# Performance work log

Hardware: AMD Instinct MI355X
Metric: run time of the kernel (lower is better)

Reference implementation:

```python
import jax, jax.numpy as jnp
import numpy as np

N = 50000   # nnodes
E = 1600000 # edges (avg degree 32)
F = 128     # nfeatures
D = 64      # output_dim
T = 10      # s2v iterations (default in n2v)


def setup_inputs() -> dict:
    key = jax.random.key(0)
    k_x, k_s, k_d, k_w1, k_w2 = jax.random.split(key, 5)
    x = jax.random.normal(k_x, (N, F), dtype=jnp.float32)
    edge_src = jax.random.randint(k_s, (E,), 0, N, dtype=jnp.int32)
    edge_dst = jax.random.randint(k_d, (E,), 0, N, dtype=jnp.int32)
    # xavier_uniform init as in reset_parameters
    s1 = float(np.sqrt(6.0 / (F + D)))
    s2 = float(np.sqrt(6.0 / (D + D)))
    W1 = jax.random.uniform(k_w1, (D, F), jnp.float32, -s1, s1)
    W2 = jax.random.uniform(k_w2, (D, D), jnp.float32, -s2, s2)
    b1 = jnp.zeros((D,), jnp.float32)
    b2 = jnp.zeros((D,), jnp.float32)
    return {"x": x, "W1": W1, "b1": b1, "W2": W2, "b2": b2,
            "edge_src": edge_src, "edge_dst": edge_dst}


def reference(x, W1, b1, W2, b2, edge_src, edge_dst):
    Wx = x @ W1.T + b1                      # [N, D]

    def step(emb, _):
        # sum of neighbor embeddings: gather sources, segment-sum into dests
        agg = jax.ops.segment_sum(emb[edge_src], edge_dst, num_segments=N)  # [N, D]
        emb_new = jax.nn.relu(Wx + agg @ W2.T + b2)
        return emb_new, None

    emb0 = jnp.zeros((N, D), dtype=x.dtype)
    emb, _ = jax.lax.scan(step, emb0, None, length=T)  # n2v
    # g2v: sum node embeddings into graph embedding
    return emb.sum(axis=0)                  # [D]
```

## Files before the change

kernel.cpp:

```cpp
#include <hip/hip_runtime.h>

#define D 64
#define F 128
#define NBMAX 256

typedef unsigned int uint;
typedef unsigned short ushort;
typedef short s16x8 __attribute__((ext_vector_type(8)));
typedef float f32x4 __attribute__((ext_vector_type(4)));

__device__ __forceinline__ float bf16lo(uint u) { return __uint_as_float(u << 16); }
__device__ __forceinline__ float bf16hi(uint u) { return __uint_as_float(u & 0xFFFF0000u); }
__device__ __forceinline__ ushort f2bf16(float f) {
    uint u = __float_as_uint(f);
    u += 0x7FFFu + ((u >> 16) & 1u);
    return (ushort)(u >> 16);
}
__device__ __forceinline__ uint pk2bf(float lo, float hi) {
    return (uint)f2bf16(lo) | ((uint)f2bf16(hi) << 16);
}
__device__ __forceinline__ float rdlane(float v, int l) {
    return __uint_as_float(__builtin_amdgcn_readlane(__float_as_uint(v), l));
}


__global__ __launch_bounds__(256) void bucket_hist(const int* __restrict__ dst,
                                                   int* __restrict__ gb, int E, int nb) {
    __shared__ int h[NBMAX];
    for (int t = threadIdx.x; t < nb; t += 256) h[t] = 0;
    __syncthreads();
    int start = blockIdx.x * 4096;
    int end   = start + 4096 < E ? start + 4096 : E;
    for (int i = start + threadIdx.x; i < end; i += 256)
        atomicAdd(&h[dst[i] >> 8], 1);
    __syncthreads();
    for (int t = threadIdx.x; t < nb; t += 256)
        if (h[t]) atomicAdd(&gb[t], h[t]);
}

__global__ void bucket_scan(const int* __restrict__ gb, int* __restrict__ gboff,
                            int* __restrict__ gcur, int nb) {
    if (threadIdx.x == 0) {
        int s = 0;
        for (int b = 0; b < nb; ++b) { gboff[b] = s; gcur[b] = s; s += gb[b]; }
        gboff[nb] = s;
    }
}

__global__ __launch_bounds__(256) void bucket_scatter(const int* __restrict__ src,
                                                      const int* __restrict__ dst,
                                                      int* __restrict__ gcur,
                                                      int* __restrict__ packed, int E, int nb) {
    __shared__ int h[NBMAX], base[NBMAX], lcur[NBMAX];
    for (int t = threadIdx.x; t < nb; t += 256) h[t] = 0;
    __syncthreads();
    int start = blockIdx.x * 4096;
    int end   = start + 4096 < E ? start + 4096 : E;
    for (int i = start + threadIdx.x; i < end; i += 256)
        atomicAdd(&h[dst[i] >> 8], 1);
    __syncthreads();
    for (int t = threadIdx.x; t < nb; t += 256) {
        base[t] = h[t] ? atomicAdd(&gcur[t], h[t]) : 0;
        lcur[t] = 0;
    }
    __syncthreads();
    for (int i = start + threadIdx.x; i < end; i += 256) {
        int d = dst[i];
        int b = d >> 8;
        int pos = base[b] + atomicAdd(&lcur[b], 1);
        packed[pos] = (src[i] << 8) | (d & 255);
    }
}

__global__ __launch_bounds__(256) void bucket_deg(const int* __restrict__ gboff,
                                                  const int* __restrict__ packed,
                                                  int* __restrict__ deg, int N) {
    __shared__ int h[NBMAX];
    int b = blockIdx.x;
    h[threadIdx.x] = 0;
    __syncthreads();
    int st = gboff[b], en = gboff[b + 1];
    for (int i = st + threadIdx.x; i < en; i += 256)
        atomicAdd(&h[packed[i] & 255], 1);
    __syncthreads();
    int node = (b << 8) + threadIdx.x;
    if (node < N) deg[node] = h[threadIdx.x];
}

__global__ __launch_bounds__(256) void bucket_fill(const int* __restrict__ gboff,
                                                   const int* __restrict__ packed,
                                                   const int* __restrict__ row_ptr,
                                                   int* __restrict__ col, int N) {
    __shared__ int lcur[NBMAX];
    int b = blockIdx.x;
    int node = (b << 8) + threadIdx.x;
    lcur[threadIdx.x] = (node < N) ? row_ptr[node] : 0;
    __syncthreads();
    int st = gboff[b], en = gboff[b + 1];
    for (int i = st + threadIdx.x; i < en; i += 256) {
        int p = packed[i];
        int pos = atomicAdd(&lcur[p & 255], 1);
        col[pos] = p >> 8;
    }
}


__global__ void count_deg_kernel(const int* __restrict__ dst, int* __restrict__ deg, int E) {
    int i = blockIdx.x * blockDim.x + threadIdx.x;
    if (i < E) atomicAdd(&deg[dst[i]], 1);
}

__global__ void fill_kernel(const int* __restrict__ src, const int* __restrict__ dst,
                            int* __restrict__ cursor, int* __restrict__ col, int E) {
    int i = blockIdx.x * blockDim.x + threadIdx.x;
    if (i < E) {
        int d_ = dst[i];
        int pos = atomicAdd(&cursor[d_], 1);
        col[pos] = src[i];
    }
}


__global__ __launch_bounds__(1024) void scan_kernel(const int* __restrict__ deg,
                                                    int* __restrict__ row_ptr, int n) {
    __shared__ int wsum[16];
    int lane = threadIdx.x & 63;
    int wid  = threadIdx.x >> 6;
    int carry = 0;
    const int CH = 4096;
    for (int base = 0; base < n; base += CH) {
        int i0 = base + (int)threadIdx.x * 4;
        int v0 = (i0     < n) ? ((deg[i0]     + 15) & ~15) : 0;
        int v1 = (i0 + 1 < n) ? ((deg[i0 + 1] + 15) & ~15) : 0;
        int v2 = (i0 + 2 < n) ? ((deg[i0 + 2] + 15) & ~15) : 0;
        int v3 = (i0 + 3 < n) ? ((deg[i0 + 3] + 15) & ~15) : 0;
        int p0 = v0, p1 = p0 + v1, p2 = p1 + v2, p3 = p2 + v3;
        int tsum = p3;
        int s = tsum;
        #pragma unroll
        for (int off = 1; off < 64; off <<= 1) {
            int t = __shfl_up(s, off);
            if (lane >= off) s += t;
        }
        if (lane == 63) wsum[wid] = s;
        __syncthreads();
        int wbase = 0, chunk_total = 0;
        #pragma unroll
        for (int w = 0; w < 16; ++w) {
            int t = wsum[w];
            chunk_total += t;
            if (w < wid) wbase += t;
        }
        __syncthreads();
        int ex = carry + wbase + (s - tsum);
        if (i0     < n) row_ptr[i0 + 1] = ex + p0;
        if (i0 + 1 < n) row_ptr[i0 + 2] = ex + p1;
        if (i0 + 2 < n) row_ptr[i0 + 3] = ex + p2;
        if (i0 + 3 < n) row_ptr[i0 + 4] = ex + p3;
        carry += chunk_total;
    }
    if (threadIdx.x == 0) row_ptr[0] = 0;
}

__global__ void pad_kernel(const int* __restrict__ row_ptr, const int* __restrict__ deg,
                           int* __restrict__ col, int N) {
    int v = blockIdx.x * blockDim.x + threadIdx.x;
    if (v < N) {
        int st = row_ptr[v] + deg[v];
        int en = row_ptr[v + 1];
        for (int k = st; k < en; ++k) col[k] = N;
    }
}


__global__ __launch_bounds__(256) void wx_mfma_kernel(const float* __restrict__ x,
                                                      const float* __restrict__ W1,
                                                      const float* __restrict__ b1,
                                                      const float* __restrict__ b2,
                                                      float* __restrict__ Wx,
                                                      ushort* __restrict__ emb, int N) {
    int lane = threadIdx.x & 63;
    int wv = blockIdx.x * 4 + (threadIdx.x >> 6);
    int nwaves = gridDim.x * 4;
    int r16 = lane & 15;
    int kg  = lane >> 4;

    s16x8 bf[4][4];
    #pragma unroll
    for (int nt = 0; nt < 4; ++nt) {
        const float* wrow = W1 + (size_t)(nt * 16 + r16) * F;
        #pragma unroll
        for (int ks = 0; ks < 4; ++ks) {
            const float4* p = reinterpret_cast<const float4*>(wrow + ks * 32 + kg * 8);
            float4 f0 = p[0], f1 = p[1];
            union { s16x8 v; uint u[4]; } t;
            t.u[0] = pk2bf(f0.x, f0.y); t.u[1] = pk2bf(f0.z, f0.w);
            t.u[2] = pk2bf(f1.x, f1.y); t.u[3] = pk2bf(f1.z, f1.w);
            bf[nt][ks] = t.v;
        }
    }
    float b1v[4], b2v[4];
    #pragma unroll
    for (int nt = 0; nt < 4; ++nt) {
        b1v[nt] = b1[nt * 16 + r16];
        b2v[nt] = b2[nt * 16 + r16];
    }

    int ntiles = (N + 15) >> 4;
    for (int tile = wv; tile < ntiles; tile += nwaves) {
        int row0 = tile << 4;
        int arow = row0 + r16;
        if (arow >= N) arow = N - 1;
        s16x8 af[4];
        #pragma unroll
        for (int ks = 0; ks < 4; ++ks) {
            const float4* p = reinterpret_cast<const float4*>(x + (size_t)arow * F + ks * 32 + kg * 8);
            float4 f0 = p[0], f1 = p[1];
            union { s16x8 v; uint u[4]; } t;
            t.u[0] = pk2bf(f0.x, f0.y); t.u[1] = pk2bf(f0.z, f0.w);
            t.u[2] = pk2bf(f1.x, f1.y); t.u[3] = pk2bf(f1.z, f1.w);
            af[ks] = t.v;
        }
        #pragma unroll
        for (int nt = 0; nt < 4; ++nt) {
            f32x4 acc = {0.f, 0.f, 0.f, 0.f};
            #pragma unroll
            for (int ks = 0; ks < 4; ++ks)
                acc = __builtin_amdgcn_mfma_f32_16x16x32_bf16(af[ks], bf[nt][ks], acc, 0, 0, 0);
            int outd = nt * 16 + r16;
            #pragma unroll
            for (int r = 0; r < 4; ++r) {
                int node = row0 + kg * 4 + r;
                if (node < N) {
                    float wxv = acc[r] + b1v[nt];
                    Wx[(size_t)node * D + outd] = wxv;
                    float e = wxv + b2v[nt];
                    emb[(size_t)node * D + outd] = f2bf16(e > 0.f ? e : 0.f);
                }
            }
        }
    }
}


template <bool LAST>
__global__ __launch_bounds__(256) void step_kernel(const ushort* __restrict__ emb_in,
                                                   ushort* __restrict__ emb_out,
                                                   const float* __restrict__ Wx,
                                                   const float* __restrict__ W2,
                                                   const float* __restrict__ b2,
                                                   const int* __restrict__ row_ptr,
                                                   const int* __restrict__ col,
                                                   float* __restrict__ out, int N) {
    __shared__ float w2t[D][D + 1];
    int t = threadIdx.x;
    #pragma unroll
    for (int i = t; i < D * D; i += 256) {
        int dd = i >> 6, kk = i & 63;
        w2t[kk][dd] = W2[i];
    }
    __syncthreads();
    int lane = t & 63, wid = t >> 6;
    float b2v = b2[lane];
    int g = lane >> 3, s = lane & 7;
    int nw = gridDim.x * 4;
    float sacc = 0.f;
    for (int v = blockIdx.x * 4 + wid; v < N; v += nw) {
        int st = row_ptr[v], en = row_ptr[v + 1];
        float a0 = 0.f, a1 = 0.f, a2 = 0.f, a3 = 0.f, a4 = 0.f, a5 = 0.f, a6 = 0.f, a7 = 0.f;
        if (st < en) {
            int u0 = col[st + g], u1 = col[st + 8 + g];
            uint4 q0 = reinterpret_cast<const uint4*>(emb_in + ((size_t)u0 << 6))[s];
            uint4 q1 = reinterpret_cast<const uint4*>(emb_in + ((size_t)u1 << 6))[s];
            int k = st + 16;
            int n0 = N, n1 = N;
            if (k < en) { n0 = col[k + g]; n1 = col[k + 8 + g]; }
            for (; k < en; k += 16) {
                uint4 p0 = reinterpret_cast<const uint4*>(emb_in + ((size_t)n0 << 6))[s];
                uint4 p1 = reinterpret_cast<const uint4*>(emb_in + ((size_t)n1 << 6))[s];
                int k2 = k + 16;
                int m0 = N, m1 = N;
                if (k2 < en) { m0 = col[k2 + g]; m1 = col[k2 + 8 + g]; }
                a0 += bf16lo(q0.x); a1 += bf16hi(q0.x);
                a2 += bf16lo(q0.y); a3 += bf16hi(q0.y);
                a4 += bf16lo(q0.z); a5 += bf16hi(q0.z);
                a6 += bf16lo(q0.w); a7 += bf16hi(q0.w);
                a0 += bf16lo(q1.x); a1 += bf16hi(q1.x);
                a2 += bf16lo(q1.y); a3 += bf16hi(q1.y);
                a4 += bf16lo(q1.z); a5 += bf16hi(q1.z);
                a6 += bf16lo(q1.w); a7 += bf16hi(q1.w);
                q0 = p0; q1 = p1; n0 = m0; n1 = m1;
            }
            a0 += bf16lo(q0.x); a1 += bf16hi(q0.x);
            a2 += bf16lo(q0.y); a3 += bf16hi(q0.y);
            a4 += bf16lo(q0.z); a5 += bf16hi(q0.z);
            a6 += bf16lo(q0.w); a7 += bf16hi(q0.w);
            a0 += bf16lo(q1.x); a1 += bf16hi(q1.x);
            a2 += bf16lo(q1.y); a3 += bf16hi(q1.y);
            a4 += bf16lo(q1.z); a5 += bf16hi(q1.z);
            a6 += bf16lo(q1.w); a7 += bf16hi(q1.w);
        }
        #pragma unroll
        for (int off = 8; off < 64; off <<= 1) {
            a0 += __shfl_xor(a0, off); a1 += __shfl_xor(a1, off);
            a2 += __shfl_xor(a2, off); a3 += __shfl_xor(a3, off);
            a4 += __shfl_xor(a4, off); a5 += __shfl_xor(a5, off);
            a6 += __shfl_xor(a6, off); a7 += __shfl_xor(a7, off);
        }
        float r = Wx[(size_t)v * D + lane] + b2v;
        #pragma unroll
        for (int kk = 0; kk < D; ++kk) {
            float av;
            switch (kk & 7) {
                case 0: av = rdlane(a0, kk >> 3); break;
                case 1: av = rdlane(a1, kk >> 3); break;
                case 2: av = rdlane(a2, kk >> 3); break;
                case 3: av = rdlane(a3, kk >> 3); break;
                case 4: av = rdlane(a4, kk >> 3); break;
                case 5: av = rdlane(a5, kk >> 3); break;
                case 6: av = rdlane(a6, kk >> 3); break;
                default: av = rdlane(a7, kk >> 3); break;
            }
            r += av * w2t[kk][lane];
        }
        float rr = r > 0.f ? r : 0.f;
        if (LAST) {
            sacc += __uint_as_float((uint)f2bf16(rr) << 16);
        } else {
            emb_out[(size_t)v * D + lane] = f2bf16(rr);
        }
    }
    if (LAST) {
        __shared__ float red[256];
        red[t] = sacc;
        __syncthreads();
        if (t < 64) {
            float sum = red[t] + red[t + 64] + red[t + 128] + red[t + 192];
            atomicAdd(&out[t], sum);
        }
    }
}

extern "C" void kernel_launch(void* const* d_in, const int* in_sizes, int n_in,
                              void* d_out, int out_size, void* d_ws, size_t ws_size,
                              hipStream_t stream) {
    const float* x    = (const float*)d_in[0];
    const float* W1   = (const float*)d_in[1];
    const float* b1   = (const float*)d_in[2];
    const float* W2   = (const float*)d_in[3];
    const float* b2   = (const float*)d_in[4];
    const int*   esrc = (const int*)d_in[5];
    const int*   edst = (const int*)d_in[6];
    int N = in_sizes[0] / F;
    int E = in_sizes[5];
    float* out = (float*)d_out;

    char* ws = (char*)d_ws;
    size_t off = 0;
    auto alloc = [&](size_t bytes) -> char* {
        char* p = ws + off;
        off += (bytes + 255) & ~(size_t)255;
        return p;
    };
    float*  Wx      = (float*)alloc((size_t)N * D * 4);
    ushort* embA    = (ushort*)alloc(((size_t)N + 1) * D * 2);
    ushort* embB    = (ushort*)alloc(((size_t)N + 1) * D * 2);
    int*    row_ptr = (int*)alloc(((size_t)N + 1) * 4);
    int*    deg     = (int*)alloc((size_t)N * 4);
    int*    col     = (int*)alloc(((size_t)E + 15 * (size_t)N) * 4);
    int*    packed  = (int*)alloc((size_t)E * 4);
    int*    gb      = (int*)alloc((NBMAX + 1) * 4);
    int*    gboff   = (int*)alloc((NBMAX + 1) * 4);
    int*    gcur    = (int*)alloc((NBMAX + 1) * 4);
    int*    cursor  = (int*)alloc((size_t)N * 4);

    hipMemsetAsync(out, 0, (size_t)out_size * 4, stream);
    hipMemsetAsync(embA + (size_t)N * D, 0, D * 2, stream);
    hipMemsetAsync(embB + (size_t)N * D, 0, D * 2, stream);

    int nb = ((N - 1) >> 8) + 1;
    int nchunks = (E + 4095) / 4096;
    if (N <= 65536) {
        hipMemsetAsync(gb, 0, (size_t)nb * 4, stream);
        bucket_hist<<<nchunks, 256, 0, stream>>>(edst, gb, E, nb);
        bucket_scan<<<1, 64, 0, stream>>>(gb, gboff, gcur, nb);
        bucket_scatter<<<nchunks, 256, 0, stream>>>(esrc, edst, gcur, packed, E, nb);
        bucket_deg<<<nb, 256, 0, stream>>>(gboff, packed, deg, N);
        scan_kernel<<<1, 1024, 0, stream>>>(deg, row_ptr, N);
        bucket_fill<<<nb, 256, 0, stream>>>(gboff, packed, row_ptr, col, N);
    } else {
        hipMemsetAsync(deg, 0, (size_t)N * 4, stream);
        count_deg_kernel<<<(E + 255) / 256, 256, 0, stream>>>(edst, deg, E);
        scan_kernel<<<1, 1024, 0, stream>>>(deg, row_ptr, N);
        hipMemcpyAsync(cursor, row_ptr, (size_t)N * 4, hipMemcpyDeviceToDevice, stream);
        fill_kernel<<<(E + 255) / 256, 256, 0, stream>>>(esrc, edst, cursor, col, E);
    }
    pad_kernel<<<(N + 255) / 256, 256, 0, stream>>>(row_ptr, deg, col, N);

    wx_mfma_kernel<<<256, 256, 0, stream>>>(x, W1, b1, b2, Wx, embA, N);

    ushort* pin = embA;
    ushort* pout = embB;
    for (int t = 1; t < 9; ++t) {
        step_kernel<false><<<2048, 256, 0, stream>>>(pin, pout, Wx, W2, b2, row_ptr, col,
                                                     out, N);
        ushort* tmp = pin; pin = pout; pout = tmp;
    }
    step_kernel<true><<<2048, 256, 0, stream>>>(pin, pout, Wx, W2, b2, row_ptr, col,
                                                out, N);
}
```

Before: 534.5 us.

## Split neighbor gather into source-half passes for cache locality

Each CSR row is partitioned by source index into a low half and a high half, each padded to 16 entries. Each iteration now runs two kernels: one gathers the low-half neighbors into an fp32 agg buffer, and the other gathers the high half, adds agg, and applies W2 and ReLU. The aim is to keep the working set of each gather pass (half the bf16 embedding table) resident in the per-XCD L2. In exchange it writes and reads a full N×64 fp32 buffer every iteration, adds padding and launches, and swaps the global atomic output reduction for per-block partials plus a final reduce kernel; the wx grid size is also raised.

```diff
diff --git a/kernel.cpp b/kernel.cpp
--- a/kernel.cpp
+++ b/kernel.cpp
@@ -22,6 +22,7 @@
 __device__ __forceinline__ float rdlane(float v, int l) {
     return __uint_as_float(__builtin_amdgcn_readlane(__float_as_uint(v), l));
 }
+__device__ __forceinline__ int ceil16(int x) { return (x + 15) & ~15; }
 
 
 __global__ __launch_bounds__(256) void bucket_hist(const int* __restrict__ dst,
@@ -87,20 +88,41 @@
     if (node < N) deg[node] = h[threadIdx.x];
 }
 
+__global__ __launch_bounds__(256) void bucket_cntlo(const int* __restrict__ gboff,
+                                                    const int* __restrict__ packed,
+                                                    int* __restrict__ cnt_lo, int N, int NH) {
+    __shared__ int h[NBMAX];
+    int b = blockIdx.x;
+    h[threadIdx.x] = 0;
+    __syncthreads();
+    int st = gboff[b], en = gboff[b + 1];
+    for (int i = st + threadIdx.x; i < en; i += 256) {
+        int p = packed[i];
+        if ((p >> 8) < NH) atomicAdd(&h[p & 255], 1);
+    }
+    __syncthreads();
+    int node = (b << 8) + threadIdx.x;
+    if (node < N) cnt_lo[node] = h[threadIdx.x];
+}
+
 __global__ __launch_bounds__(256) void bucket_fill(const int* __restrict__ gboff,
                                                    const int* __restrict__ packed,
                                                    const int* __restrict__ row_ptr,
-                                                   int* __restrict__ col, int N) {
-    __shared__ int lcur[NBMAX];
+                                                   const int* __restrict__ cnt_lo,
+                                                   int* __restrict__ col, int N, int NH) {
+    __shared__ int lcur_lo[NBMAX], lcur_hi[NBMAX];
     int b = blockIdx.x;
     int node = (b << 8) + threadIdx.x;
-    lcur[threadIdx.x] = (node < N) ? row_ptr[node] : 0;
+    lcur_lo[threadIdx.x] = (node < N) ? row_ptr[node] : 0;
+    lcur_hi[threadIdx.x] = (node < N) ? row_ptr[node] + ceil16(cnt_lo[node]) : 0;
     __syncthreads();
     int st = gboff[b], en = gboff[b + 1];
     for (int i = st + threadIdx.x; i < en; i += 256) {
         int p = packed[i];
-        int pos = atomicAdd(&lcur[p & 255], 1);
-        col[pos] = p >> 8;
+        int s = p >> 8;
+        int pos = (s < NH) ? atomicAdd(&lcur_lo[p & 255], 1)
+                           : atomicAdd(&lcur_hi[p & 255], 1);
+        col[pos] = s;
     }
 }
 
@@ -110,18 +132,33 @@
     if (i < E) atomicAdd(&deg[dst[i]], 1);
 }
 
-__global__ void fill_kernel(const int* __restrict__ src, const int* __restrict__ dst,
-                            int* __restrict__ cursor, int* __restrict__ col, int E) {
+__global__ void cntlo_global_kernel(const int* __restrict__ src, const int* __restrict__ dst,
+                                    int* __restrict__ cnt_lo, int E, int NH) {
+    int i = blockIdx.x * blockDim.x + threadIdx.x;
+    if (i < E && src[i] < NH) atomicAdd(&cnt_lo[dst[i]], 1);
+}
+
+__global__ void mkcur_kernel(const int* __restrict__ row_ptr, const int* __restrict__ cnt_lo,
+                             int* __restrict__ cur_lo, int* __restrict__ cur_hi, int N) {
+    int v = blockIdx.x * blockDim.x + threadIdx.x;
+    if (v < N) { cur_lo[v] = row_ptr[v]; cur_hi[v] = row_ptr[v] + ceil16(cnt_lo[v]); }
+}
+
+__global__ void fill2_kernel(const int* __restrict__ src, const int* __restrict__ dst,
+                             int* __restrict__ cur_lo, int* __restrict__ cur_hi,
+                             int* __restrict__ col, int E, int NH) {
     int i = blockIdx.x * blockDim.x + threadIdx.x;
     if (i < E) {
         int d_ = dst[i];
-        int pos = atomicAdd(&cursor[d_], 1);
-        col[pos] = src[i];
+        int s = src[i];
+        int pos = (s < NH) ? atomicAdd(&cur_lo[d_], 1) : atomicAdd(&cur_hi[d_], 1);
+        col[pos] = s;
     }
 }
 
 
 __global__ __launch_bounds__(1024) void scan_kernel(const int* __restrict__ deg,
+                                                    const int* __restrict__ cnt_lo,
                                                     int* __restrict__ row_ptr, int n) {
     __shared__ int wsum[16];
     int lane = threadIdx.x & 63;
@@ -130,10 +167,11 @@
     const int CH = 4096;
     for (int base = 0; base < n; base += CH) {
         int i0 = base + (int)threadIdx.x * 4;
-        int v0 = (i0     < n) ? ((deg[i0]     + 15) & ~15) : 0;
-        int v1 = (i0 + 1 < n) ? ((deg[i0 + 1] + 15) & ~15) : 0;
-        int v2 = (i0 + 2 < n) ? ((deg[i0 + 2] + 15) & ~15) : 0;
-        int v3 = (i0 + 3 < n) ? ((deg[i0 + 3] + 15) & ~15) : 0;
+        int v0 = 0, v1 = 0, v2 = 0, v3 = 0;
+        if (i0     < n) { int c = cnt_lo[i0];     v0 = ceil16(c) + ceil16(deg[i0]     - c); }
+        if (i0 + 1 < n) { int c = cnt_lo[i0 + 1]; v1 = ceil16(c) + ceil16(deg[i0 + 1] - c); }
+        if (i0 + 2 < n) { int c = cnt_lo[i0 + 2]; v2 = ceil16(c) + ceil16(deg[i0 + 2] - c); }
+        if (i0 + 3 < n) { int c = cnt_lo[i0 + 3]; v3 = ceil16(c) + ceil16(deg[i0 + 3] - c); }
         int p0 = v0, p1 = p0 + v1, p2 = p1 + v2, p3 = p2 + v3;
         int tsum = p3;
         int s = tsum;
@@ -163,12 +201,16 @@
 }
 
 __global__ void pad_kernel(const int* __restrict__ row_ptr, const int* __restrict__ deg,
-                           int* __restrict__ col, int N) {
+                           const int* __restrict__ cnt_lo, int* __restrict__ col, int N) {
     int v = blockIdx.x * blockDim.x + threadIdx.x;
     if (v < N) {
-        int st = row_ptr[v] + deg[v];
-        int en = row_ptr[v + 1];
-        for (int k = st; k < en; ++k) col[k] = N;
+        int rp = row_ptr[v];
+        int cl = cnt_lo[v], ch = deg[v] - cl;
+        int cl16 = ceil16(cl);
+        for (int k = rp + cl; k < rp + cl16; ++k) col[k] = N;
+        int hbase = rp + cl16;
+        int ch16 = ceil16(ch);
+        for (int k = hbase + ch; k < hbase + ch16; ++k) col[k] = N;
     }
 }
 
@@ -243,15 +285,85 @@
 }
 
 
+#define GATHER_SECTION(pin_, st_, en_)                                              \
+    if ((st_) < (en_)) {                                                            \
+        int u0 = col[(st_) + g], u1 = col[(st_) + 8 + g];                           \
+        uint4 q0 = reinterpret_cast<const uint4*>((pin_) + ((size_t)u0 << 6))[s];   \
+        uint4 q1 = reinterpret_cast<const uint4*>((pin_) + ((size_t)u1 << 6))[s];   \
+        int k = (st_) + 16;                                                         \
+        int n0 = N, n1 = N;                                                         \
+        if (k < (en_)) { n0 = col[k + g]; n1 = col[k + 8 + g]; }                    \
+        for (; k < (en_); k += 16) {                                                \
+            uint4 p0 = reinterpret_cast<const uint4*>((pin_) + ((size_t)n0 << 6))[s]; \
+            uint4 p1 = reinterpret_cast<const uint4*>((pin_) + ((size_t)n1 << 6))[s]; \
+            int k2 = k + 16;                                                        \
+            int m0 = N, m1 = N;                                                     \
+            if (k2 < (en_)) { m0 = col[k2 + g]; m1 = col[k2 + 8 + g]; }             \
+            a0 += bf16lo(q0.x); a1 += bf16hi(q0.x);                                 \
+            a2 += bf16lo(q0.y); a3 += bf16hi(q0.y);                                 \
+            a4 += bf16lo(q0.z); a5 += bf16hi(q0.z);                                 \
+            a6 += bf16lo(q0.w); a7 += bf16hi(q0.w);                                 \
+            a0 += bf16lo(q1.x); a1 += bf16hi(q1.x);                                 \
+            a2 += bf16lo(q1.y); a3 += bf16hi(q1.y);                                 \
+            a4 += bf16lo(q1.z); a5 += bf16hi(q1.z);                                 \
+            a6 += bf16lo(q1.w); a7 += bf16hi(q1.w);                                 \
+            q0 = p0; q1 = p1; n0 = m0; n1 = m1;                                     \
+        }                                                                           \
+        a0 += bf16lo(q0.x); a1 += bf16hi(q0.x);                                     \
+        a2 += bf16lo(q0.y); a3 += bf16hi(q0.y);                                     \
+        a4 += bf16lo(q0.z); a5 += bf16hi(q0.z);                                     \
+        a6 += bf16lo(q0.w); a7 += bf16hi(q0.w);                                     \
+        a0 += bf16lo(q1.x); a1 += bf16hi(q1.x);                                     \
+        a2 += bf16lo(q1.y); a3 += bf16hi(q1.y);                                     \
+        a4 += bf16lo(q1.z); a5 += bf16hi(q1.z);                                     \
+        a6 += bf16lo(q1.w); a7 += bf16hi(q1.w);                                     \
+    }
+
+#define XOR_REDUCE()                                                                \
+    _Pragma("unroll")                                                               \
+    for (int off = 8; off < 64; off <<= 1) {                                        \
+        a0 += __shfl_xor(a0, off); a1 += __shfl_xor(a1, off);                       \
+        a2 += __shfl_xor(a2, off); a3 += __shfl_xor(a3, off);                       \
+        a4 += __shfl_xor(a4, off); a5 += __shfl_xor(a5, off);                       \
+        a6 += __shfl_xor(a6, off); a7 += __shfl_xor(a7, off);                       \
+    }
+
+
+__global__ __launch_bounds__(256) void gather_lo_kernel(const ushort* __restrict__ emb_in,
+                                                        float* __restrict__ agg,
+                                                        const int* __restrict__ row_ptr,
+                                                        const int* __restrict__ col,
+                                                        const int* __restrict__ cnt_lo, int N) {
+    int t = threadIdx.x;
+    int lane = t & 63, wid = t >> 6;
+    int g = lane >> 3, s = lane & 7;
+    int nw = gridDim.x * 4;
+    for (int v = blockIdx.x * 4 + wid; v < N; v += nw) {
+        int st = row_ptr[v];
+        int en = st + ceil16(cnt_lo[v]);
+        float a0 = 0.f, a1 = 0.f, a2 = 0.f, a3 = 0.f, a4 = 0.f, a5 = 0.f, a6 = 0.f, a7 = 0.f;
+        GATHER_SECTION(emb_in, st, en)
+        XOR_REDUCE()
+        if (g == 0) {
+            float* ap = agg + (size_t)v * D + s * 8;
+            *reinterpret_cast<float4*>(ap)     = (float4){a0, a1, a2, a3};
+            *reinterpret_cast<float4*>(ap + 4) = (float4){a4, a5, a6, a7};
+        }
+    }
+}
+
+
 template <bool LAST>
-__global__ __launch_bounds__(256) void step_kernel(const ushort* __restrict__ emb_in,
-                                                   ushort* __restrict__ emb_out,
-                                                   const float* __restrict__ Wx,
-                                                   const float* __restrict__ W2,
-                                                   const float* __restrict__ b2,
-                                                   const int* __restrict__ row_ptr,
-                                                   const int* __restrict__ col,
-                                                   float* __restrict__ out, int N) {
+__global__ __launch_bounds__(256) void gather_hi_finish_kernel(const ushort* __restrict__ emb_in,
+                                                               const float* __restrict__ agg,
+                                                               ushort* __restrict__ emb_out,
+                                                               const float* __restrict__ Wx,
+                                                               const float* __restrict__ W2,
+                                                               const float* __restrict__ b2,
+                                                               const int* __restrict__ row_ptr,
+                                                               const int* __restrict__ col,
+                                                               const int* __restrict__ cnt_lo,
+                                                               float* __restrict__ partial, int N) {
     __shared__ float w2t[D][D + 1];
     int t = threadIdx.x;
     #pragma unroll
@@ -266,47 +378,28 @@
     int nw = gridDim.x * 4;
     float sacc = 0.f;
     for (int v = blockIdx.x * 4 + wid; v < N; v += nw) {
-        int st = row_ptr[v], en = row_ptr[v + 1];
-        float a0 = 0.f, a1 = 0.f, a2 = 0.f, a3 = 0.f, a4 = 0.f, a5 = 0.f, a6 = 0.f, a7 = 0.f;
-        if (st < en) {
-            int u0 = col[st + g], u1 = col[st + 8 + g];
-            uint4 q0 = reinterpret_cast<const uint4*>(emb_in + ((size_t)u0 << 6))[s];
-            uint4 q1 = reinterpret_cast<const uint4*>(emb_in + ((size_t)u1 << 6))[s];
-            int k = st + 16;
-            int n0 = N, n1 = N;
-            if (k < en) { n0 = col[k + g]; n1 = col[k + 8 + g]; }
-            for (; k < en; k += 16) {
-                uint4 p0 = reinterpret_cast<const uint4*>(emb_in + ((size_t)n0 << 6))[s];
-                uint4 p1 = reinterpret_cast<const uint4*>(emb_in + ((size_t)n1 << 6))[s];
-                int k2 = k + 16;
-                int m0 = N, m1 = N;
-                if (k2 < en) { m0 = col[k2 + g]; m1 = col[k2 + 8 + g]; }
-                a0 += bf16lo(q0.x); a1 += bf16hi(q0.x);
-                a2 += bf16lo(q0.y); a3 += bf16hi(q0.y);
-                a4 += bf16lo(q0.z); a5 += bf16hi(q0.z);
-                a6 += bf16lo(q0.w); a7 += bf16hi(q0.w);
-                a0 += bf16lo(q1.x); a1 += bf16hi(q1.x);
-                a2 += bf16lo(q1.y); a3 += bf16hi(q1.y);
-                a4 += bf16lo(q1.z); a5 += bf16hi(q1.z);
-                a6 += bf16lo(q1.w); a7 += bf16hi(q1.w);
-                q0 = p0; q1 = p1; n0 = m0; n1 = m1;
-            }
-            a0 += bf16lo(q0.x); a1 += bf16hi(q0.x);
-            a2 += bf16lo(q0.y); a3 += bf16hi(q0.y);
-            a4 += bf16lo(q0.z); a5 += bf16hi(q0.z);
-            a6 += bf16lo(q0.w); a7 += bf16hi(q0.w);
-            a0 += bf16lo(q1.x); a1 += bf16hi(q1.x);
-            a2 += bf16lo(q1.y); a3 += bf16hi(q1.y);
-            a4 += bf16lo(q1.z); a5 += bf16hi(q1.z);
-            a6 += bf16lo(q1.w); a7 += bf16hi(q1.w);
-        }
-        #pragma unroll
-        for (int off = 8; off < 64; off <<= 1) {
-            a0 += __shfl_xor(a0, off); a1 += __shfl_xor(a1, off);
-            a2 += __shfl_xor(a2, off); a3 += __shfl_xor(a3, off);
-            a4 += __shfl_xor(a4, off); a5 += __shfl_xor(a5, off);
-            a6 += __shfl_xor(a6, off); a7 += __shfl_xor(a7, off);
-        }
+        int rp = row_ptr[v];
+        int st = rp + ceil16(cnt_lo[v]);
+        int en = row_ptr[v + 1];
+        float a0, a1, a2, a3, a4, a5, a6, a7;
+        {
+            const float* ap = agg + (size_t)v * D + s * 8;
+            float4 p0 = *reinterpret_cast<const float4*>(ap);
+            float4 p1 = *reinterpret_cast<const float4*>(ap + 4);
+            a0 = p0.x; a1 = p0.y; a2 = p0.z; a3 = p0.w;
+            a4 = p1.x; a5 = p1.y; a6 = p1.z; a7 = p1.w;
+        }
+        float h0 = 0.f, h1 = 0.f, h2 = 0.f, h3 = 0.f, h4 = 0.f, h5 = 0.f, h6 = 0.f, h7 = 0.f;
+        {
+            float b0 = a0, b1 = a1, b2_ = a2, b3 = a3, b4 = a4, b5 = a5, b6 = a6, b7 = a7;
+            a0 = 0.f; a1 = 0.f; a2 = 0.f; a3 = 0.f; a4 = 0.f; a5 = 0.f; a6 = 0.f; a7 = 0.f;
+            GATHER_SECTION(emb_in, st, en)
+            XOR_REDUCE()
+            h0 = b0; h1 = b1; h2 = b2_; h3 = b3; h4 = b4; h5 = b5; h6 = b6; h7 = b7;
+        }
+        a0 += h0; a1 += h1; a2 += h2; a3 += h3;
+        a4 += h4; a5 += h5; a6 += h6; a7 += h7;
+
         float r = Wx[(size_t)v * D + lane] + b2v;
         #pragma unroll
         for (int kk = 0; kk < D; ++kk) {
@@ -336,9 +429,23 @@
         __syncthreads();
         if (t < 64) {
             float sum = red[t] + red[t + 64] + red[t + 128] + red[t + 192];
-            atomicAdd(&out[t], sum);
-        }
-    }
+            partial[(size_t)blockIdx.x * 64 + t] = sum;
+        }
+    }
+}
+
+__global__ __launch_bounds__(256) void final_reduce_kernel(const float* __restrict__ partial,
+                                                           float* __restrict__ out, int nblocks) {
+    __shared__ float red[256];
+    int t = threadIdx.x;
+    int d = t & 63, q = t >> 6;
+    float acc = 0.f;
+    for (int b = q; b < nblocks; b += 4)
+        acc += partial[(size_t)b * 64 + d];
+    red[t] = acc;
+    __syncthreads();
+    if (t < 64)
+        out[t] = red[t] + red[t + 64] + red[t + 128] + red[t + 192];
 }
 
 extern "C" void kernel_launch(void* const* d_in, const int* in_sizes, int n_in,
@@ -353,6 +460,7 @@
     const int*   edst = (const int*)d_in[6];
     int N = in_sizes[0] / F;
     int E = in_sizes[5];
+    int NH = N >> 1;
     float* out = (float*)d_out;
 
     char* ws = (char*)d_ws;
@@ -365,16 +473,19 @@
     float*  Wx      = (float*)alloc((size_t)N * D * 4);
     ushort* embA    = (ushort*)alloc(((size_t)N + 1) * D * 2);
     ushort* embB    = (ushort*)alloc(((size_t)N + 1) * D * 2);
+    float*  agg     = (float*)alloc((size_t)N * D * 4);
     int*    row_ptr = (int*)alloc(((size_t)N + 1) * 4);
     int*    deg     = (int*)alloc((size_t)N * 4);
-    int*    col     = (int*)alloc(((size_t)E + 15 * (size_t)N) * 4);
+    int*    cnt_lo  = (int*)alloc((size_t)N * 4);
+    int*    col     = (int*)alloc(((size_t)E + 31 * (size_t)N) * 4);
     int*    packed  = (int*)alloc((size_t)E * 4);
+    float*  partial = (float*)alloc((size_t)2048 * 64 * 4);
     int*    gb      = (int*)alloc((NBMAX + 1) * 4);
     int*    gboff   = (int*)alloc((NBMAX + 1) * 4);
     int*    gcur    = (int*)alloc((NBMAX + 1) * 4);
-    int*    cursor  = (int*)alloc((size_t)N * 4);
-
-    hipMemsetAsync(out, 0, (size_t)out_size * 4, stream);
+    int*    cur_lo  = (int*)alloc((size_t)N * 4);
+    int*    cur_hi  = (int*)alloc((size_t)N * 4);
+
     hipMemsetAsync(embA + (size_t)N * D, 0, D * 2, stream);
     hipMemsetAsync(embB + (size_t)N * D, 0, D * 2, stream);
 
@@ -386,26 +497,34 @@
         bucket_scan<<<1, 64, 0, stream>>>(gb, gboff, gcur, nb);
         bucket_scatter<<<nchunks, 256, 0, stream>>>(esrc, edst, gcur, packed, E, nb);
         bucket_deg<<<nb, 256, 0, stream>>>(gboff, packed, deg, N);
-        scan_kernel<<<1, 1024, 0, stream>>>(deg, row_ptr, N);
-        bucket_fill<<<nb, 256, 0, stream>>>(gboff, packed, row_ptr, col, N);
+        bucket_cntlo<<<nb, 256, 0, stream>>>(gboff, packed, cnt_lo, N, NH);
+        scan_kernel<<<1, 1024, 0, stream>>>(deg, cnt_lo, row_ptr, N);
+        bucket_fill<<<nb, 256, 0, stream>>>(gboff, packed, row_ptr, cnt_lo, col, N, NH);
     } else {
         hipMemsetAsync(deg, 0, (size_t)N * 4, stream);
+        hipMemsetAsync(cnt_lo, 0, (size_t)N * 4, stream);
         count_deg_kernel<<<(E + 255) / 256, 256, 0, stream>>>(edst, deg, E);
-        scan_kernel<<<1, 1024, 0, stream>>>(deg, row_ptr, N);
-        hipMemcpyAsync(cursor, row_ptr, (size_t)N * 4, hipMemcpyDeviceToDevice, stream);
-        fill_kernel<<<(E + 255) / 256, 256, 0, stream>>>(esrc, edst, cursor, col, E);
-    }
-    pad_kernel<<<(N + 255) / 256, 256, 0, stream>>>(row_ptr, deg, col, N);
-
-    wx_mfma_kernel<<<256, 256, 0, stream>>>(x, W1, b1, b2, Wx, embA, N);
+        cntlo_global_kernel<<<(E + 255) / 256, 256, 0, stream>>>(esrc, edst, cnt_lo, E, NH);
+        scan_kernel<<<1, 1024, 0, stream>>>(deg, cnt_lo, row_ptr, N);
+        mkcur_kernel<<<(N + 255) / 256, 256, 0, stream>>>(row_ptr, cnt_lo, cur_lo, cur_hi, N);
+        fill2_kernel<<<(E + 255) / 256, 256, 0, stream>>>(esrc, edst, cur_lo, cur_hi, col, E, NH);
+    }
+    pad_kernel<<<(N + 255) / 256, 256, 0, stream>>>(row_ptr, deg, cnt_lo, col, N);
+
+    wx_mfma_kernel<<<1024, 256, 0, stream>>>(x, W1, b1, b2, Wx, embA, N);
 
     ushort* pin = embA;
     ushort* pout = embB;
     for (int t = 1; t < 9; ++t) {
-        step_kernel<false><<<2048, 256, 0, stream>>>(pin, pout, Wx, W2, b2, row_ptr, col,
-                                                     out, N);
+        gather_lo_kernel<<<2048, 256, 0, stream>>>(pin, agg, row_ptr, col, cnt_lo, N);
+        gather_hi_finish_kernel<false><<<2048, 256, 0, stream>>>(pin, agg, pout, Wx, W2, b2,
+                                                                 row_ptr, col, cnt_lo,
+                                                                 partial, N);
         ushort* tmp = pin; pin = pout; pout = tmp;
     }
-    step_kernel<true><<<2048, 256, 0, stream>>>(pin, pout, Wx, W2, b2, row_ptr, col,
-                                                out, N);
-}
+    gather_lo_kernel<<<2048, 256, 0, stream>>>(pin, agg, row_ptr, col, cnt_lo, N);
+    gather_hi_finish_kernel<true><<<2048, 256, 0, stream>>>(pin, agg, pout, Wx, W2, b2,
+                                                            row_ptr, col, cnt_lo,
+                                                            partial, N);
+    final_reduce_kernel<<<1, 256, 0, stream>>>(partial, out, 2048);
+}
```

After: 770.8 us. 1.44x slower.
